# Kernel tuning notes

Measured on AMD Instinct MI355X. Metric: run time of the kernel, lower is better.

## Reference

```python
import jax, jax.numpy as jnp
import numpy as np

SMOOTH = 1e-6
K = 64  # num_selection_features


def setup_inputs() -> dict:
    key = jax.random.key(0)
    kx, kw, kb = jax.random.split(key, 3)
    x = jax.random.normal(kx, (8, 256, 128, 128), dtype=jnp.float32)
    # 1x1 conv: Conv2d(K, 1) -> weight [1, K, 1, 1]; store as [K] and scalar bias
    w = jax.random.normal(kw, (K,), dtype=jnp.float32) * (1.0 / np.sqrt(K))
    b = jax.random.normal(kb, (1,), dtype=jnp.float32) * 0.01
    return {"x": x, "w": w, "b": b}


def reference(x, w, b):
    B, C, H, W = x.shape
    s = jax.nn.sigmoid(x)
    uncertainty = -s * jnp.log(s + SMOOTH)           # [B,C,H,W]
    score = jnp.mean(uncertainty, axis=(2, 3))       # [B,C]
    # topk smallest -> top_k of negated score
    _, idx = jax.lax.top_k(-score, K)                # [B,K]
    selected = jnp.take_along_axis(x, idx[:, :, None, None], axis=1)  # [B,K,H,W]
    # 1x1 conv (K->1) + sigmoid
    attn = jax.nn.sigmoid(jnp.einsum('bkhw,k->bhw', selected, w) + b[0])  # [B,H,W]
    return x * attn[:, None, :, :]
```

## Files before the change

kernel.cpp:

```cpp
#include <hip/hip_runtime.h>

constexpr int B  = 8;
constexpr int C  = 256;
constexpr int HW = 128 * 128;
constexpr int K  = 64;

__device__ __forceinline__ float uncert_rank(float v) {
    float t = __expf(-v);
    float a = 1.0f + t;
    return __log2f(a) * __builtin_amdgcn_rcpf(a);
}

__global__ __launch_bounds__(256) void score_kernel(const float* __restrict__ x,
                                                    float* __restrict__ score) {
    const int plane = blockIdx.x;
    const float4* xp = (const float4*)(x + (size_t)plane * HW);
    const int t = threadIdx.x;

    float acc = 0.0f;
#pragma unroll
    for (int i = 0; i < 16; ++i) {
        float4 v = xp[t + i * 256];
        acc += uncert_rank(v.x) + uncert_rank(v.y) + uncert_rank(v.z) + uncert_rank(v.w);
    }
#pragma unroll
    for (int off = 32; off > 0; off >>= 1) acc += __shfl_down(acc, off, 64);

    __shared__ float smem[4];
    if ((t & 63) == 0) smem[t >> 6] = acc;
    __syncthreads();
    if (t == 0) score[plane] = smem[0] + smem[1] + smem[2] + smem[3];
}

__global__ __launch_bounds__(256, 2) void attn_mul_kernel(const float* __restrict__ x,
                                                          const float* __restrict__ score,
                                                          const float* __restrict__ w,
                                                          const float* __restrict__ bias,
                                                          float* __restrict__ out) {
    const int b     = blockIdx.x >> 6;
    const int chunk = blockIdx.x & 63;
    const int t     = threadIdx.x;

    __shared__ float sc[C];
    __shared__ float ws[K];
    __shared__ int   chs[K];
    __shared__ int   unch[C - K];

    sc[t] = score[b * C + t];
    if (t < K) ws[t] = w[t];
    __syncthreads();

    {
        const float my = sc[t];
        int rank = 0;
#pragma unroll 8
        for (int j = 0; j < C; ++j) {
            float o = sc[j];
            rank += (o < my) || (o == my && j < t);
        }
        if (rank < K) chs[rank] = t;
        else          unch[rank - K] = t;
    }
    __syncthreads();

    const int p = chunk * 256 + t;
    const float* xb = x + (size_t)b * C * HW;
    float*       ob = out + (size_t)b * C * HW;

    float st[K];
    float a = 0.f;
#pragma unroll
    for (int k = 0; k < K; ++k) {
        float v = xb[(size_t)chs[k] * HW + p];
        st[k] = v;
        a += ws[k] * v;
    }
    const float sg = __builtin_amdgcn_rcpf(1.0f + __expf(-(a + bias[0])));

#pragma unroll
    for (int k = 0; k < K; ++k) {
        __builtin_nontemporal_store(st[k] * sg, &ob[(size_t)chs[k] * HW + p]);
    }

#pragma unroll 8
    for (int j = 0; j < C - K; ++j) {
        const size_t idx = (size_t)unch[j] * HW + p;
        __builtin_nontemporal_store(xb[idx] * sg, &ob[idx]);
    }
}

extern "C" void kernel_launch(void* const* d_in, const int* in_sizes, int n_in,
                              void* d_out, int out_size, void* d_ws, size_t ws_size,
                              hipStream_t stream) {
    const float* x    = (const float*)d_in[0];
    const float* w    = (const float*)d_in[1];
    const float* bias = (const float*)d_in[2];
    float* out = (float*)d_out;

    float* score = (float*)d_ws;

    score_kernel<<<B * C, 256, 0, stream>>>(x, score);
    attn_mul_kernel<<<B * 64, 256, 0, stream>>>(x, score, w, bias, out);
}
```

Before: 258.3 us.

## Split attention computation and broadcast multiply into separate kernels

```diff
diff --git a/kernel.cpp b/kernel.cpp
--- a/kernel.cpp
+++ b/kernel.cpp
@@ -4,6 +4,8 @@
 constexpr int C  = 256;
 constexpr int HW = 128 * 128;
 constexpr int K  = 64;
+
+typedef float nfloat4 __attribute__((ext_vector_type(4)));
 
 __device__ __forceinline__ float uncert_rank(float v) {
     float t = __expf(-v);
@@ -32,11 +34,11 @@
     if (t == 0) score[plane] = smem[0] + smem[1] + smem[2] + smem[3];
 }
 
-__global__ __launch_bounds__(256, 2) void attn_mul_kernel(const float* __restrict__ x,
-                                                          const float* __restrict__ score,
-                                                          const float* __restrict__ w,
-                                                          const float* __restrict__ bias,
-                                                          float* __restrict__ out) {
+__global__ __launch_bounds__(256) void attn_kernel(const float* __restrict__ x,
+                                                   const float* __restrict__ score,
+                                                   const float* __restrict__ w,
+                                                   const float* __restrict__ bias,
+                                                   float* __restrict__ attn) {
     const int b     = blockIdx.x >> 6;
     const int chunk = blockIdx.x & 63;
     const int t     = threadIdx.x;
@@ -44,7 +46,6 @@
     __shared__ float sc[C];
     __shared__ float ws[K];
     __shared__ int   chs[K];
-    __shared__ int   unch[C - K];
 
     sc[t] = score[b * C + t];
     if (t < K) ws[t] = w[t];
@@ -59,33 +60,34 @@
             rank += (o < my) || (o == my && j < t);
         }
         if (rank < K) chs[rank] = t;
-        else          unch[rank - K] = t;
     }
     __syncthreads();
 
     const int p = chunk * 256 + t;
     const float* xb = x + (size_t)b * C * HW;
-    float*       ob = out + (size_t)b * C * HW;
 
-    float st[K];
     float a = 0.f;
 #pragma unroll
     for (int k = 0; k < K; ++k) {
-        float v = xb[(size_t)chs[k] * HW + p];
-        st[k] = v;
-        a += ws[k] * v;
+        a += ws[k] * xb[(size_t)chs[k] * HW + p];
     }
-    const float sg = __builtin_amdgcn_rcpf(1.0f + __expf(-(a + bias[0])));
+    attn[b * HW + p] = __builtin_amdgcn_rcpf(1.0f + __expf(-(a + bias[0])));
+}
 
-#pragma unroll
-    for (int k = 0; k < K; ++k) {
-        __builtin_nontemporal_store(st[k] * sg, &ob[(size_t)chs[k] * HW + p]);
-    }
+__global__ __launch_bounds__(256) void mul_kernel(const float* __restrict__ x,
+                                                  const float* __restrict__ attn,
+                                                  float* __restrict__ out) {
+    const float4*  x4 = (const float4*)x;
+    const float4*  a4 = (const float4*)attn;
+    nfloat4*       o4 = (nfloat4*)out;
+    constexpr size_t N4     = (size_t)B * C * HW / 4;
+    const size_t     stride = (size_t)gridDim.x * blockDim.x;
 
-#pragma unroll 8
-    for (int j = 0; j < C - K; ++j) {
-        const size_t idx = (size_t)unch[j] * HW + p;
-        __builtin_nontemporal_store(xb[idx] * sg, &ob[idx]);
+    for (size_t i = (size_t)blockIdx.x * blockDim.x + threadIdx.x; i < N4; i += stride) {
+        float4 v = x4[i];
+        float4 a = a4[((i >> 20) << 12) | (i & 4095)];
+        nfloat4 o = {v.x * a.x, v.y * a.y, v.z * a.z, v.w * a.w};
+        __builtin_nontemporal_store(o, &o4[i]);
     }
 }
 
@@ -97,8 +99,11 @@
     const float* bias = (const float*)d_in[2];
     float* out = (float*)d_out;
 
-    float* score = (float*)d_ws;
+    char* ws = (char*)d_ws;
+    float* score = (float*)ws;
+    float* attn  = (float*)(ws + 16384);
 
     score_kernel<<<B * C, 256, 0, stream>>>(x, score);
-    attn_mul_kernel<<<B * 64, 256, 0, stream>>>(x, score, w, bias, out);
+    attn_kernel<<<B * 64, 256, 0, stream>>>(x, score, w, bias, attn);
+    mul_kernel<<<2048, 256, 0, stream>>>(x, attn, out);
 }
```

Result: slower. 276.9 us (+7.2%).

## Split channel selection into its own kernel and double attn_mul grid

Applied to the files above, without the earlier changes.

```diff
diff --git a/kernel.cpp b/kernel.cpp
--- a/kernel.cpp
+++ b/kernel.cpp
@@ -4,6 +4,7 @@
 constexpr int C  = 256;
 constexpr int HW = 128 * 128;
 constexpr int K  = 64;
+constexpr int U  = C - K;
 
 __device__ __forceinline__ float uncert_rank(float v) {
     float t = __expf(-v);
@@ -32,59 +33,82 @@
     if (t == 0) score[plane] = smem[0] + smem[1] + smem[2] + smem[3];
 }
 
-__global__ __launch_bounds__(256, 2) void attn_mul_kernel(const float* __restrict__ x,
-                                                          const float* __restrict__ score,
-                                                          const float* __restrict__ w,
+__global__ __launch_bounds__(256) void select_kernel(const float* __restrict__ score,
+                                                     const float* __restrict__ w,
+                                                     int* __restrict__ asel,
+                                                     float* __restrict__ awt,
+                                                     int* __restrict__ aunsel) {
+    const int b = blockIdx.x;
+    const int t = threadIdx.x;
+    __shared__ float sc[C];
+    __shared__ int   flagv[C];
+    __shared__ float wl[K];
+
+    sc[t] = score[b * C + t];
+    if (t < K) wl[t] = w[t];
+    __syncthreads();
+
+    const float my = sc[t];
+    int rank = 0;
+#pragma unroll 8
+    for (int j = 0; j < C; ++j) {
+        float o = sc[j];
+        rank += (o < my) || (o == my && j < t);
+    }
+    const int selected = rank < K;
+    flagv[t] = selected;
+    __syncthreads();
+
+    int pos = 0;
+#pragma unroll 8
+    for (int j = 0; j < C; ++j) pos += (j < t) && (flagv[j] == selected);
+
+    if (selected) { asel[b * K + pos] = t; awt[b * K + pos] = wl[rank]; }
+    else          { aunsel[b * U + pos] = t; }
+}
+
+__global__ __launch_bounds__(256, 4) void attn_mul_kernel(const float* __restrict__ x,
+                                                          const int* __restrict__ asel,
+                                                          const float* __restrict__ awt,
+                                                          const int* __restrict__ aunsel,
                                                           const float* __restrict__ bias,
                                                           float* __restrict__ out) {
-    const int b     = blockIdx.x >> 6;
-    const int chunk = blockIdx.x & 63;
+    const int b     = blockIdx.x >> 7;
+    const int r     = blockIdx.x & 127;
+    const int chunk = r >> 1;
+    const int h     = r & 1;
     const int t     = threadIdx.x;
 
-    __shared__ float sc[C];
-    __shared__ float ws[K];
     __shared__ int   chs[K];
-    __shared__ int   unch[C - K];
-
-    sc[t] = score[b * C + t];
-    if (t < K) ws[t] = w[t];
-    __syncthreads();
-
-    {
-        const float my = sc[t];
-        int rank = 0;
-#pragma unroll 8
-        for (int j = 0; j < C; ++j) {
-            float o = sc[j];
-            rank += (o < my) || (o == my && j < t);
-        }
-        if (rank < K) chs[rank] = t;
-        else          unch[rank - K] = t;
-    }
+    __shared__ float wk[K];
+    __shared__ int   un[U];
+    if (t < K) { chs[t] = asel[b * K + t]; wk[t] = awt[b * K + t]; }
+    if (t < U) { un[t]  = aunsel[b * U + t]; }
     __syncthreads();
 
     const int p = chunk * 256 + t;
     const float* xb = x + (size_t)b * C * HW;
     float*       ob = out + (size_t)b * C * HW;
 
-    float st[K];
+    float st[K / 2];
     float a = 0.f;
 #pragma unroll
     for (int k = 0; k < K; ++k) {
         float v = xb[(size_t)chs[k] * HW + p];
-        st[k] = v;
-        a += ws[k] * v;
+        if ((k >> 5) == h) st[k & 31] = v;
+        a += wk[k] * v;
     }
     const float sg = __builtin_amdgcn_rcpf(1.0f + __expf(-(a + bias[0])));
 
 #pragma unroll
-    for (int k = 0; k < K; ++k) {
-        __builtin_nontemporal_store(st[k] * sg, &ob[(size_t)chs[k] * HW + p]);
+    for (int j = 0; j < K / 2; ++j) {
+        __builtin_nontemporal_store(st[j] * sg, &ob[(size_t)chs[h * 32 + j] * HW + p]);
     }
 
-#pragma unroll 8
-    for (int j = 0; j < C - K; ++j) {
-        const size_t idx = (size_t)unch[j] * HW + p;
+    const int jb = h * 96;
+#pragma unroll 16
+    for (int j = 0; j < U / 2; ++j) {
+        const size_t idx = (size_t)un[jb + j] * HW + p;
         __builtin_nontemporal_store(xb[idx] * sg, &ob[idx]);
     }
 }
@@ -97,8 +121,13 @@
     const float* bias = (const float*)d_in[2];
     float* out = (float*)d_out;
 
-    float* score = (float*)d_ws;
+    char* ws = (char*)d_ws;
+    float* score  = (float*)ws;
+    int*   asel   = (int*)(ws + 8192);
+    float* awt    = (float*)(ws + 10240);
+    int*   aunsel = (int*)(ws + 12288);
 
     score_kernel<<<B * C, 256, 0, stream>>>(x, score);
-    attn_mul_kernel<<<B * 64, 256, 0, stream>>>(x, score, w, bias, out);
+    select_kernel<<<B, 256, 0, stream>>>(score, w, asel, awt, aunsel);
+    attn_mul_kernel<<<B * 128, 256, 0, stream>>>(x, asel, awt, aunsel, bias, out);
 }
```

Result: slower. 268.1 us (+3.8%).

## Vectorize attn_mul with float4 and split channel reduction across wavefronts

Applied to the files above, without the earlier changes.

```diff
diff --git a/kernel.cpp b/kernel.cpp
--- a/kernel.cpp
+++ b/kernel.cpp
@@ -1,9 +1,13 @@
 #include <hip/hip_runtime.h>
 
-constexpr int B  = 8;
-constexpr int C  = 256;
-constexpr int HW = 128 * 128;
-constexpr int K  = 64;
+constexpr int B   = 8;
+constexpr int C   = 256;
+constexpr int HW  = 128 * 128;
+constexpr int HW4 = HW / 4;
+constexpr int K   = 64;
+constexpr int U   = C - K;
+
+typedef float nfloat4 __attribute__((ext_vector_type(4)));
 
 __device__ __forceinline__ float uncert_rank(float v) {
     float t = __expf(-v);
@@ -40,11 +44,15 @@
     const int b     = blockIdx.x >> 6;
     const int chunk = blockIdx.x & 63;
     const int t     = threadIdx.x;
+    const int sub   = t >> 6;
+    const int col   = t & 63;
 
     __shared__ float sc[C];
     __shared__ float ws[K];
     __shared__ int   chs[K];
-    __shared__ int   unch[C - K];
+    __shared__ int   unch[U];
+    __shared__ float4 part[4][64];
+    __shared__ float4 attnS[64];
 
     sc[t] = score[b * C + t];
     if (t < K) ws[t] = w[t];
@@ -63,29 +71,51 @@
     }
     __syncthreads();
 
-    const int p = chunk * 256 + t;
-    const float* xb = x + (size_t)b * C * HW;
-    float*       ob = out + (size_t)b * C * HW;
+    const int col4 = chunk * 64 + col;
+    const float4* xb4 = (const float4*)(x + (size_t)b * C * HW);
+    float*        obf = out + (size_t)b * C * HW;
 
-    float st[K];
-    float a = 0.f;
+    float4 st[16];
+    float ax = 0.f, ay = 0.f, az = 0.f, aw = 0.f;
 #pragma unroll
-    for (int k = 0; k < K; ++k) {
-        float v = xb[(size_t)chs[k] * HW + p];
-        st[k] = v;
-        a += ws[k] * v;
+    for (int j = 0; j < 16; ++j) {
+        const int k = sub * 16 + j;
+        float4 v = xb4[(size_t)chs[k] * HW4 + col4];
+        st[j] = v;
+        const float wk = ws[k];
+        ax += wk * v.x; ay += wk * v.y; az += wk * v.z; aw += wk * v.w;
     }
-    const float sg = __builtin_amdgcn_rcpf(1.0f + __expf(-(a + bias[0])));
+    { float4 p; p.x = ax; p.y = ay; p.z = az; p.w = aw; part[sub][col] = p; }
+    __syncthreads();
+
+    if (t < 64) {
+        float4 p0 = part[0][t], p1 = part[1][t], p2 = part[2][t], p3 = part[3][t];
+        const float b0 = bias[0];
+        float4 a4;
+        a4.x = __builtin_amdgcn_rcpf(1.0f + __expf(-(p0.x + p1.x + p2.x + p3.x + b0)));
+        a4.y = __builtin_amdgcn_rcpf(1.0f + __expf(-(p0.y + p1.y + p2.y + p3.y + b0)));
+        a4.z = __builtin_amdgcn_rcpf(1.0f + __expf(-(p0.z + p1.z + p2.z + p3.z + b0)));
+        a4.w = __builtin_amdgcn_rcpf(1.0f + __expf(-(p0.w + p1.w + p2.w + p3.w + b0)));
+        attnS[t] = a4;
+    }
+    __syncthreads();
+    const float4 a4 = attnS[col];
 
 #pragma unroll
-    for (int k = 0; k < K; ++k) {
-        __builtin_nontemporal_store(st[k] * sg, &ob[(size_t)chs[k] * HW + p]);
+    for (int j = 0; j < 16; ++j) {
+        const int k = sub * 16 + j;
+        nfloat4 o = {st[j].x * a4.x, st[j].y * a4.y, st[j].z * a4.z, st[j].w * a4.w};
+        __builtin_nontemporal_store(o,
+            (nfloat4*)(obf + ((size_t)chs[k] * HW4 + col4) * 4));
     }
 
 #pragma unroll 8
-    for (int j = 0; j < C - K; ++j) {
-        const size_t idx = (size_t)unch[j] * HW + p;
-        __builtin_nontemporal_store(xb[idx] * sg, &ob[idx]);
+    for (int j = 0; j < U / 4; ++j) {
+        const int ch = unch[sub * (U / 4) + j];
+        const size_t idx = (size_t)ch * HW4 + col4;
+        float4 v = xb4[idx];
+        nfloat4 o = {v.x * a4.x, v.y * a4.y, v.z * a4.z, v.w * a4.w};
+        __builtin_nontemporal_store(o, (nfloat4*)(obf + idx * 4));
     }
 }
 
```

New measurement: 257.7 us. About the same (-0.3%).
